# Kernel tuning notes

Measured on AMD Instinct MI355X. Metric: run time of the kernel, lower is better.

## Reference

```python
import jax, jax.numpy as jnp
import numpy as np
from jax.ops import segment_sum

N = 100000   # total nodes
M = 50000    # propagated subset size (len(index))
E = 600000   # edges over the subset graph
D = 128      # embedding_size
EPS = 1e-8
N_LAYERS = 3  # self.LayerNums


def setup_inputs() -> dict:
    key = jax.random.key(0)
    ks = jax.random.split(key, 12)
    features = jax.random.normal(ks[0], (N, D), dtype=jnp.float32)
    index = jnp.arange(M, dtype=jnp.int64)  # subset of nodes that get propagated
    edge_row = jax.random.randint(ks[1], (E,), 0, M, dtype=jnp.int64)
    edge_col = jax.random.randint(ks[2], (E,), 0, M, dtype=jnp.int64)
    edge_val = jax.random.uniform(ks[3], (E,), dtype=jnp.float32)
    # MLP prediction weights: D -> D//2 -> D//4 -> D//6 -> 1 (last no bias)
    def xavier(k, fan_in, fan_out):
        lim = jnp.sqrt(6.0 / (fan_in + fan_out)).astype(jnp.float32)
        return jax.random.uniform(k, (fan_in, fan_out), jnp.float32, -lim, lim)
    W1 = xavier(ks[4], D, D // 2); b1 = jnp.zeros((D // 2,), jnp.float32)
    W2 = xavier(ks[5], D // 2, D // 4); b2 = jnp.zeros((D // 4,), jnp.float32)
    W3 = xavier(ks[6], D // 4, D // 6); b3 = jnp.zeros((D // 6,), jnp.float32)
    W4 = xavier(ks[7], D // 6, 1)
    return {"features": features, "index": index, "edge_row": edge_row,
            "edge_col": edge_col, "edge_val": edge_val,
            "W1": W1, "b1": b1, "W2": W2, "b2": b2, "W3": W3, "b3": b3, "W4": W4}


def _gcn_layer(features, index, row, col, val):
    # symmetric normalization: d = rowsum(A)+eps; A' = d^-1/2 A d^-1/2
    deg = segment_sum(val, row, num_segments=M)
    d_inv_sqrt = jax.lax.rsqrt(deg + EPS)
    nval = val * d_inv_sqrt[row] * d_inv_sqrt[col]
    sub = features[index]                      # [M, D] subset_features
    msg = sub[col] * nval[:, None]             # [E, D]
    out = segment_sum(msg, row, num_segments=M)  # spmm -> [M, D]
    # new_features[index] = out; untouched rows keep original features
    return features.at[index].set(out)


def reference(features, index, edge_row, edge_col, edge_val,
              W1, b1, W2, b2, W3, b3, W4):
    x = features
    for _ in range(N_LAYERS):
        x = _gcn_layer(x, index, edge_row, edge_col, edge_val)
    # MLP prediction head (eval mode: dropout off), LeakyReLU slope 0.01
    h = jax.nn.leaky_relu(x @ W1 + b1, 0.01)
    h = jax.nn.leaky_relu(h @ W2 + b2, 0.01)
    h = jax.nn.leaky_relu(h @ W3 + b3, 0.01)
    return jax.nn.sigmoid(h @ W4)              # [N, 1]
```

## Files before the change

### kernel.cpp

```cpp
#include <hip/hip_runtime.h>
#include <math.h>

#define NN 100000
#define MM 50000
#define EE 600000
#define DD 128
#define NB 196
#define NNP 100096

typedef short bf16x8 __attribute__((ext_vector_type(8)));
typedef float f32x4 __attribute__((ext_vector_type(4)));

__device__ __forceinline__ float bl(unsigned u) { return __uint_as_float(u << 16); }
__device__ __forceinline__ float bh(unsigned u) { return __uint_as_float(u & 0xFFFF0000u); }
__device__ __forceinline__ unsigned rne(float f) {
    unsigned u = __float_as_uint(f);
    return (u + 0x7FFFu + ((u >> 16) & 1u)) >> 16;
}
__device__ __forceinline__ unsigned pk2(float a, float b) { return rne(a) | (rne(b) << 16); }

__device__ __forceinline__ void fmab8(float v, uint4 u, float* a) {
    a[0] = fmaf(v, bl(u.x), a[0]); a[1] = fmaf(v, bh(u.x), a[1]);
    a[2] = fmaf(v, bl(u.y), a[2]); a[3] = fmaf(v, bh(u.y), a[3]);
    a[4] = fmaf(v, bl(u.z), a[4]); a[5] = fmaf(v, bh(u.z), a[5]);
    a[6] = fmaf(v, bl(u.w), a[6]); a[7] = fmaf(v, bh(u.w), a[7]);
}

__device__ __forceinline__ void fma21(float h, const float* wrow, float* a) {
    #pragma unroll
    for (int j = 0; j < 21; ++j) a[j] = fmaf(h, wrow[j], a[j]);
}

__global__ void deg_count_kernel(const int* __restrict__ row, const float* __restrict__ val,
                                 unsigned long long* __restrict__ dcpack,
                                 int* __restrict__ slot, int* __restrict__ invidx) {
    int e = blockIdx.x * 256 + threadIdx.x;
    if (e < NN) invidx[e] = -1;
    if (e < EE) {
        int r = row[e];
        unsigned long long add = (1ULL << 44) | (unsigned long long)(val[e] * 4294967296.0f);
        unsigned long long old = atomicAdd(&dcpack[r], add);
        slot[e] = (int)(old >> 44);
    }
}

__global__ void fused_setup_kernel(const unsigned long long* __restrict__ dcpack,
                                   float* __restrict__ dis,
                                   const int* __restrict__ index, int* __restrict__ invidx,
                                   int* __restrict__ cnt, int* __restrict__ partial,
                                   int* __restrict__ bsum) {
    __shared__ int ws[4];
    int tid = threadIdx.x, lane = tid & 63, w = tid >> 6;
    int i = blockIdx.x * 256 + tid;
    int v = 0;
    if (i < MM) {
        unsigned long long pkv = dcpack[i];
        v = (int)(pkv >> 44);
        float dsum = (float)(pkv & ((1ULL << 44) - 1)) * (1.0f / 4294967296.0f);
        dis[i] = rsqrtf(dsum + 1e-8f);
        invidx[index[i]] = i;
        cnt[i] = v;
    }
    int x = v;
    #pragma unroll
    for (int off = 1; off < 64; off <<= 1) {
        int t = __shfl_up(x, off, 64);
        if (lane >= off) x += t;
    }
    if (lane == 63) ws[w] = x;
    __syncthreads();
    int add = 0;
    for (int q = 0; q < w; ++q) add += ws[q];
    x += add;
    if (i < MM) partial[i] = x;
    if (tid == 255) bsum[blockIdx.x] = x;
}

__global__ void scanB_kernel(const int* __restrict__ bsum, int* __restrict__ boff) {
    int lane = threadIdx.x;
    int carry = 0;
    for (int base = 0; base < NB; base += 64) {
        int v = (base + lane < NB) ? bsum[base + lane] : 0;
        int x = v;
        #pragma unroll
        for (int off = 1; off < 64; off <<= 1) {
            int t = __shfl_up(x, off, 64);
            if (lane >= off) x += t;
        }
        if (base + lane < NB) boff[base + lane] = carry + x - v;
        carry += __shfl(x, 63);
    }
}

__global__ void scanC_kernel(const int* __restrict__ partial, const int* __restrict__ cnt,
                             const int* __restrict__ boff, int* __restrict__ rowptr) {
    int i = blockIdx.x * 256 + threadIdx.x;
    if (i < MM) rowptr[i] = partial[i] - cnt[i] + boff[i >> 8];
    if (i == 0) rowptr[MM] = EE;
}

__global__ void scatter_kernel(const int* __restrict__ row, const int* __restrict__ col,
                               const float* __restrict__ val, const float* __restrict__ dis,
                               const int* __restrict__ rowptr, const int* __restrict__ slot,
                               int* __restrict__ col_s, float* __restrict__ val_s) {
    int e = blockIdx.x * 256 + threadIdx.x;
    if (e < EE) {
        int r = row[e], c = col[e];
        int pos = rowptr[r] + slot[e];
        col_s[pos] = c;
        val_s[pos] = val[e] * dis[r] * dis[c];
    }
}

__global__ void cvt_kernel(const float* __restrict__ feat, const int* __restrict__ index,
                           const int* __restrict__ invidx,
                           unsigned* __restrict__ X0b, unsigned* __restrict__ Xfull,
                           const float* __restrict__ W1, const float* __restrict__ W2,
                           unsigned* __restrict__ W1b, unsigned* __restrict__ W2b) {
    int i = blockIdx.x * 256 + threadIdx.x;
    int n = i >> 6, u = i & 63;
    if (n < NN && invidx[n] < 0) {
        float2 f = ((const float2*)feat)[(size_t)n * 64 + u];
        Xfull[(size_t)n * 64 + u] = pk2(f.x, f.y);
    }
    if (i < MM * 64) {
        int idx = index[n];
        float2 f = ((const float2*)feat)[(size_t)idx * 64 + u];
        X0b[i] = pk2(f.x, f.y);
    }
    if (i < 4096) {
        int j = i >> 6, kp = i & 63;
        W1b[i] = pk2(W1[(2 * kp) * 64 + j], W1[(2 * kp + 1) * 64 + j]);
    } else if (i < 5120) {
        int t = i - 4096;
        int j = t >> 5, kp = t & 31;
        W2b[t] = pk2(W2[(2 * kp) * 32 + j], W2[(2 * kp + 1) * 32 + j]);
    }
}

__global__ __launch_bounds__(256) void spmm_kernel(
    const int* __restrict__ rowptr, const int* __restrict__ cols,
    const float* __restrict__ vals, const unsigned short* __restrict__ X,
    unsigned short* __restrict__ Y, const int* __restrict__ remap) {
    int lane = threadIdx.x & 63;
    int wid = threadIdx.x >> 6;
    int g = lane >> 4, sub = lane & 15;
    int r = blockIdx.x * 16 + wid * 4 + g;
    bool valid = (r < MM);
    int rc = valid ? r : (MM - 1);
    int s = rowptr[rc], e = rowptr[rc + 1];
    const uint4* __restrict__ X4 = (const uint4*)X;
    float a[8] = {0.f, 0.f, 0.f, 0.f, 0.f, 0.f, 0.f, 0.f};
    for (int base = s; base < e; base += 16) {
        int cnt = min(16, e - base);
        int c = 0; float v = 0.f;
        if (sub < cnt) { c = cols[base + sub]; v = vals[base + sub]; }
        int j = 0;
        for (; j + 4 <= cnt; j += 4) {
            int c0 = __shfl(c, g * 16 + j);     float v0 = __shfl(v, g * 16 + j);
            int c1 = __shfl(c, g * 16 + j + 1); float v1 = __shfl(v, g * 16 + j + 1);
            int c2 = __shfl(c, g * 16 + j + 2); float v2 = __shfl(v, g * 16 + j + 2);
            int c3 = __shfl(c, g * 16 + j + 3); float v3 = __shfl(v, g * 16 + j + 3);
            uint4 u0 = X4[(size_t)c0 * 16 + sub];
            uint4 u1 = X4[(size_t)c1 * 16 + sub];
            uint4 u2 = X4[(size_t)c2 * 16 + sub];
            uint4 u3 = X4[(size_t)c3 * 16 + sub];
            fmab8(v0, u0, a);
            fmab8(v1, u1, a);
            fmab8(v2, u2, a);
            fmab8(v3, u3, a);
        }
        for (; j < cnt; ++j) {
            int cc = __shfl(c, g * 16 + j); float vv = __shfl(v, g * 16 + j);
            uint4 u0 = X4[(size_t)cc * 16 + sub];
            fmab8(vv, u0, a);
        }
    }
    if (valid) {
        int dst = remap ? remap[rc] : rc;
        uint4 o;
        o.x = pk2(a[0], a[1]); o.y = pk2(a[2], a[3]);
        o.z = pk2(a[4], a[5]); o.w = pk2(a[6], a[7]);
        ((uint4*)Y)[(size_t)dst * 16 + sub] = o;
    }
}

__global__ __launch_bounds__(256) void mlp_kernel(
    const unsigned* __restrict__ Xfull,
    const unsigned* __restrict__ W1b, const float* __restrict__ b1,
    const unsigned* __restrict__ W2b, const float* __restrict__ b2,
    const float* __restrict__ W3, const float* __restrict__ b3,
    const float* __restrict__ W4, float* __restrict__ out) {
    __shared__ float hls[4 * 1088];
    int tid = threadIdx.x;
    int lane = tid & 63, w = tid >> 6;
    int p = lane & 15, q = lane >> 4;
    float* hw = hls + w * 1088;
    int nb = blockIdx.x * 64;
    int node = nb + w * 16 + p;

    bf16x8 af[4];
    #pragma unroll
    for (int kc = 0; kc < 4; ++kc) {
        uint4 u = *(const uint4*)(Xfull + (size_t)node * 64 + kc * 16 + q * 4);
        af[kc] = *(const bf16x8*)&u;
    }
    f32x4 acc[4];
    #pragma unroll
    for (int jt = 0; jt < 4; ++jt) {
        float bv = b1[jt * 16 + p];
        acc[jt][0] = bv; acc[jt][1] = bv; acc[jt][2] = bv; acc[jt][3] = bv;
    }
    #pragma unroll
    for (int jt = 0; jt < 4; ++jt) {
        #pragma unroll
        for (int kc = 0; kc < 4; ++kc) {
            uint4 u = *(const uint4*)(W1b + (jt * 16 + p) * 64 + kc * 16 + q * 4);
            bf16x8 bf = *(const bf16x8*)&u;
            acc[jt] = __builtin_amdgcn_mfma_f32_16x16x32_bf16(af[kc], bf, acc[jt], 0, 0, 0);
        }
    }
    #pragma unroll
    for (int jt = 0; jt < 4; ++jt) {
        #pragma unroll
        for (int r = 0; r < 4; ++r) {
            float v = acc[jt][r];
            v = v > 0.f ? v : 0.01f * v;
            hw[(q * 4 + r) * 68 + jt * 16 + p] = v;
        }
    }
    bf16x8 a2f[2];
    #pragma unroll
    for (int kc = 0; kc < 2; ++kc) {
        const float* hp = hw + p * 68 + kc * 32 + q * 8;
        f32x4 v0 = *(const f32x4*)hp;
        f32x4 v1 = *(const f32x4*)(hp + 4);
        uint4 uu = make_uint4(pk2(v0[0], v0[1]), pk2(v0[2], v0[3]),
                              pk2(v1[0], v1[1]), pk2(v1[2], v1[3]));
        a2f[kc] = *(const bf16x8*)&uu;
    }
    f32x4 acc2[2];
    #pragma unroll
    for (int jt = 0; jt < 2; ++jt) {
        float bv = b2[jt * 16 + p];
        acc2[jt][0] = bv; acc2[jt][1] = bv; acc2[jt][2] = bv; acc2[jt][3] = bv;
        #pragma unroll
        for (int kc = 0; kc < 2; ++kc) {
            uint4 u = *(const uint4*)(W2b + (jt * 16 + p) * 32 + kc * 16 + q * 4);
            bf16x8 bf = *(const bf16x8*)&u;
            acc2[jt] = __builtin_amdgcn_mfma_f32_16x16x32_bf16(a2f[kc], bf, acc2[jt], 0, 0, 0);
        }
    }
    #pragma unroll
    for (int jt = 0; jt < 2; ++jt) {
        #pragma unroll
        for (int r = 0; r < 4; ++r) {
            float v = acc2[jt][r];
            v = v > 0.f ? v : 0.01f * v;
            hw[(q * 4 + r) * 36 + jt * 16 + p] = v;
        }
    }
    float a3[21];
    #pragma unroll
    for (int j = 0; j < 21; ++j) a3[j] = b3[j];
    #pragma unroll 4
    for (int k = 0; k < 32; ++k) {
        float hk = hw[p * 36 + k];
        fma21(hk, W3 + k * 21, a3);
    }
    float s = 0.f;
    #pragma unroll
    for (int j = 0; j < 21; ++j) {
        float vj = a3[j] > 0.f ? a3[j] : 0.01f * a3[j];
        s = fmaf(vj, W4[j], s);
    }
    if (q == 0) {
        int n = nb + w * 16 + p;
        if (n < NN) out[n] = 1.f / (1.f + expf(-s));
    }
}

extern "C" void kernel_launch(void* const* d_in, const int* in_sizes, int n_in,
                              void* d_out, int out_size, void* d_ws, size_t ws_size,
                              hipStream_t stream) {
    const float* feat = (const float*)d_in[0];
    const int*   index = (const int*)d_in[1];
    const int*   erow = (const int*)d_in[2];
    const int*   ecol = (const int*)d_in[3];
    const float* evalp = (const float*)d_in[4];
    const float* W1 = (const float*)d_in[5];
    const float* b1 = (const float*)d_in[6];
    const float* W2 = (const float*)d_in[7];
    const float* b2 = (const float*)d_in[8];
    const float* W3 = (const float*)d_in[9];
    const float* b3 = (const float*)d_in[10];
    const float* W4 = (const float*)d_in[11];
    float* out = (float*)d_out;

    char* ws = (char*)d_ws;
    size_t off = 0;
    auto alloc = [&](size_t bytes) -> void* {
        void* p = ws + off;
        off += (bytes + 255) & ~(size_t)255;
        return p;
    };
    unsigned long long* dcpack = (unsigned long long*)alloc((size_t)MM * 8);
    float* dis     = (float*)alloc((size_t)MM * 4);
    int*   cnt     = (int*)  alloc((size_t)MM * 4);
    int*   rowptr  = (int*)  alloc((size_t)(MM + 1) * 4);
    int*   partial = (int*)  alloc((size_t)MM * 4);
    int*   bsum    = (int*)  alloc((size_t)NB * 4);
    int*   boff    = (int*)  alloc((size_t)NB * 4);
    int*   slot    = (int*)  alloc((size_t)EE * 4);
    int*   col_s   = (int*)  alloc((size_t)EE * 4);
    float* val_s   = (float*)alloc((size_t)EE * 4);
    int*   invidx  = (int*)  alloc((size_t)NN * 4);
    unsigned* W1b  = (unsigned*)alloc(4096 * 4);
    unsigned* W2b  = (unsigned*)alloc(1024 * 4);
    unsigned*       X0b   = (unsigned*)      alloc((size_t)MM * DD * 2);
    unsigned short* Xa    = (unsigned short*)alloc((size_t)MM * DD * 2);
    unsigned short* Xb    = (unsigned short*)alloc((size_t)MM * DD * 2);
    unsigned*       Xfull = (unsigned*)      alloc((size_t)NNP * DD * 2);

    hipMemsetAsync(dcpack, 0, (size_t)MM * 8, stream);

    deg_count_kernel<<<(EE + 255) / 256, 256, 0, stream>>>(erow, evalp, dcpack, slot, invidx);
    fused_setup_kernel<<<NB, 256, 0, stream>>>(dcpack, dis, index, invidx, cnt, partial, bsum);
    scanB_kernel<<<1, 64, 0, stream>>>(bsum, boff);
    scanC_kernel<<<(MM + 255) / 256, 256, 0, stream>>>(partial, cnt, boff, rowptr);
    scatter_kernel<<<(EE + 255) / 256, 256, 0, stream>>>(erow, ecol, evalp, dis,
                                                         rowptr, slot, col_s, val_s);
    cvt_kernel<<<(NN * 64 + 255) / 256, 256, 0, stream>>>(feat, index, invidx, X0b, Xfull,
                                                          W1, W2, W1b, W2b);

    spmm_kernel<<<(MM + 15) / 16, 256, 0, stream>>>(rowptr, col_s, val_s,
                                                    (const unsigned short*)X0b, Xa, nullptr);
    spmm_kernel<<<(MM + 15) / 16, 256, 0, stream>>>(rowptr, col_s, val_s, Xa, Xb, nullptr);
    spmm_kernel<<<(MM + 15) / 16, 256, 0, stream>>>(rowptr, col_s, val_s, Xb,
                                                    (unsigned short*)Xfull, index);

    mlp_kernel<<<(NNP + 63) / 64, 256, 0, stream>>>(Xfull, W1b, b1, W2b, b2,
                                                    W3, b3, W4, out);
}
```

Baseline: 270.6 us.

## Sort rows by degree and pad CSR rows to multiples of four

Rebuilds the CSR setup as a counting sort of rows by degree, using per-block degree histograms and a bin scan. Each row's edge list is padded to a multiple of four with zeroed entries. The SpMM then handles rows in descending-degree order, so groups sharing a wavefront have similar trip counts, and it loads columns and values as int4/float4 without shuffles or tail loops. The cost is larger zero-filled edge buffers, a wider memset and an extra sort pass. Rows with degree 255 or more all share one histogram bin.

```diff
diff --git a/kernel.cpp b/kernel.cpp
--- a/kernel.cpp
+++ b/kernel.cpp
@@ -7,6 +7,7 @@
 #define DD 128
 #define NB 196
 #define NNP 100096
+#define EE4 750000
 
 typedef short bf16x8 __attribute__((ext_vector_type(8)));
 typedef float f32x4 __attribute__((ext_vector_type(4)));
@@ -47,66 +48,87 @@
 __global__ void fused_setup_kernel(const unsigned long long* __restrict__ dcpack,
                                    float* __restrict__ dis,
                                    const int* __restrict__ index, int* __restrict__ invidx,
-                                   int* __restrict__ cnt, int* __restrict__ partial,
-                                   int* __restrict__ bsum) {
-    __shared__ int ws[4];
-    int tid = threadIdx.x, lane = tid & 63, w = tid >> 6;
+                                   int* __restrict__ cnt, int* __restrict__ blockhist) {
+    __shared__ int lh[256];
+    int tid = threadIdx.x;
     int i = blockIdx.x * 256 + tid;
-    int v = 0;
+    lh[tid] = 0;
+    __syncthreads();
     if (i < MM) {
         unsigned long long pkv = dcpack[i];
-        v = (int)(pkv >> 44);
+        int v = (int)(pkv >> 44);
         float dsum = (float)(pkv & ((1ULL << 44) - 1)) * (1.0f / 4294967296.0f);
         dis[i] = rsqrtf(dsum + 1e-8f);
         invidx[index[i]] = i;
         cnt[i] = v;
-    }
-    int x = v;
-    #pragma unroll
-    for (int off = 1; off < 64; off <<= 1) {
-        int t = __shfl_up(x, off, 64);
-        if (lane >= off) x += t;
-    }
-    if (lane == 63) ws[w] = x;
+        atomicAdd(&lh[min(v, 255)], 1);
+    }
     __syncthreads();
-    int add = 0;
-    for (int q = 0; q < w; ++q) add += ws[q];
-    x += add;
-    if (i < MM) partial[i] = x;
-    if (tid == 255) bsum[blockIdx.x] = x;
-}
-
-__global__ void scanB_kernel(const int* __restrict__ bsum, int* __restrict__ boff) {
+    blockhist[tid * NB + blockIdx.x] = lh[tid];
+}
+
+__global__ void scan_bins_kernel(const int* __restrict__ blockhist,
+                                 int* __restrict__ blockoff, int* __restrict__ total) {
+    int d = blockIdx.x;
     int lane = threadIdx.x;
     int carry = 0;
     for (int base = 0; base < NB; base += 64) {
-        int v = (base + lane < NB) ? bsum[base + lane] : 0;
+        int b = base + lane;
+        int v = (b < NB) ? blockhist[d * NB + b] : 0;
         int x = v;
         #pragma unroll
         for (int off = 1; off < 64; off <<= 1) {
             int t = __shfl_up(x, off, 64);
             if (lane >= off) x += t;
         }
-        if (base + lane < NB) boff[base + lane] = carry + x - v;
+        if (b < NB) blockoff[d * NB + b] = carry + x - v;
         carry += __shfl(x, 63);
     }
-}
-
-__global__ void scanC_kernel(const int* __restrict__ partial, const int* __restrict__ cnt,
-                             const int* __restrict__ boff, int* __restrict__ rowptr) {
-    int i = blockIdx.x * 256 + threadIdx.x;
-    if (i < MM) rowptr[i] = partial[i] - cnt[i] + boff[i >> 8];
-    if (i == 0) rowptr[MM] = EE;
+    if (lane == 0) total[d] = carry;
+}
+
+__global__ void sort_rows_kernel(const int* __restrict__ cnt, const int* __restrict__ blockoff,
+                                 const int* __restrict__ total, const int* __restrict__ index,
+                                 int4* __restrict__ meta, int* __restrict__ row_s4) {
+    __shared__ int lh[256], sbin[256], spad[256], ws[8];
+    int tid = threadIdx.x, lane = tid & 63, w = tid >> 6;
+    lh[tid] = 0;
+    int t = total[tid];
+    int v1 = t, v2 = t * ((tid + 3) & ~3);
+    int x1 = v1, x2 = v2;
+    #pragma unroll
+    for (int off = 1; off < 64; off <<= 1) {
+        int t1 = __shfl_up(x1, off, 64);
+        int t2 = __shfl_up(x2, off, 64);
+        if (lane >= off) { x1 += t1; x2 += t2; }
+    }
+    if (lane == 63) { ws[w] = x1; ws[4 + w] = x2; }
+    __syncthreads();
+    int a1 = 0, a2 = 0;
+    for (int q = 0; q < w; ++q) { a1 += ws[q]; a2 += ws[4 + q]; }
+    sbin[tid] = a1 + x1 - v1;
+    spad[tid] = a2 + x2 - v2;
+    __syncthreads();
+    int i = blockIdx.x * 256 + tid;
+    if (i < MM) {
+        int d = cnt[i], c = min(d, 255);
+        int lrank = atomicAdd(&lh[c], 1);
+        int k = blockoff[c * NB + blockIdx.x] + lrank;
+        int spos = sbin[c] + k;
+        int s4 = spad[c] + k * ((d + 3) & ~3);
+        meta[MM - 1 - spos] = make_int4(s4, d, i, index[i]);
+        row_s4[i] = s4;
+    }
 }
 
 __global__ void scatter_kernel(const int* __restrict__ row, const int* __restrict__ col,
                                const float* __restrict__ val, const float* __restrict__ dis,
-                               const int* __restrict__ rowptr, const int* __restrict__ slot,
+                               const int* __restrict__ row_s4, const int* __restrict__ slot,
                                int* __restrict__ col_s, float* __restrict__ val_s) {
     int e = blockIdx.x * 256 + threadIdx.x;
     if (e < EE) {
         int r = row[e], c = col[e];
-        int pos = rowptr[r] + slot[e];
+        int pos = row_s4[r] + slot[e];
         col_s[pos] = c;
         val_s[pos] = val[e] * dis[r] * dis[c];
     }
@@ -139,49 +161,38 @@
 }
 
 __global__ __launch_bounds__(256) void spmm_kernel(
-    const int* __restrict__ rowptr, const int* __restrict__ cols,
+    const int4* __restrict__ meta, const int* __restrict__ cols,
     const float* __restrict__ vals, const unsigned short* __restrict__ X,
-    unsigned short* __restrict__ Y, const int* __restrict__ remap) {
+    unsigned short* __restrict__ Y, int use_remap) {
     int lane = threadIdx.x & 63;
     int wid = threadIdx.x >> 6;
     int g = lane >> 4, sub = lane & 15;
-    int r = blockIdx.x * 16 + wid * 4 + g;
-    bool valid = (r < MM);
-    int rc = valid ? r : (MM - 1);
-    int s = rowptr[rc], e = rowptr[rc + 1];
+    int ri = blockIdx.x * 16 + wid * 4 + g;
+    bool valid = (ri < MM);
+    int rc = valid ? ri : (MM - 1);
+    int4 mt = meta[rc];
+    int s = mt.x, d = mt.y;
     const uint4* __restrict__ X4 = (const uint4*)X;
     float a[8] = {0.f, 0.f, 0.f, 0.f, 0.f, 0.f, 0.f, 0.f};
-    for (int base = s; base < e; base += 16) {
-        int cnt = min(16, e - base);
-        int c = 0; float v = 0.f;
-        if (sub < cnt) { c = cols[base + sub]; v = vals[base + sub]; }
-        int j = 0;
-        for (; j + 4 <= cnt; j += 4) {
-            int c0 = __shfl(c, g * 16 + j);     float v0 = __shfl(v, g * 16 + j);
-            int c1 = __shfl(c, g * 16 + j + 1); float v1 = __shfl(v, g * 16 + j + 1);
-            int c2 = __shfl(c, g * 16 + j + 2); float v2 = __shfl(v, g * 16 + j + 2);
-            int c3 = __shfl(c, g * 16 + j + 3); float v3 = __shfl(v, g * 16 + j + 3);
-            uint4 u0 = X4[(size_t)c0 * 16 + sub];
-            uint4 u1 = X4[(size_t)c1 * 16 + sub];
-            uint4 u2 = X4[(size_t)c2 * 16 + sub];
-            uint4 u3 = X4[(size_t)c3 * 16 + sub];
-            fmab8(v0, u0, a);
-            fmab8(v1, u1, a);
-            fmab8(v2, u2, a);
-            fmab8(v3, u3, a);
-        }
-        for (; j < cnt; ++j) {
-            int cc = __shfl(c, g * 16 + j); float vv = __shfl(v, g * 16 + j);
-            uint4 u0 = X4[(size_t)cc * 16 + sub];
-            fmab8(vv, u0, a);
-        }
+    int e4 = s + d;
+    for (int base = s; base < e4; base += 4) {
+        int4 c4 = *(const int4*)(cols + base);
+        float4 v4 = *(const float4*)(vals + base);
+        uint4 u0 = X4[c4.x * 16 + sub];
+        uint4 u1 = X4[c4.y * 16 + sub];
+        uint4 u2 = X4[c4.z * 16 + sub];
+        uint4 u3 = X4[c4.w * 16 + sub];
+        fmab8(v4.x, u0, a);
+        fmab8(v4.y, u1, a);
+        fmab8(v4.z, u2, a);
+        fmab8(v4.w, u3, a);
     }
     if (valid) {
-        int dst = remap ? remap[rc] : rc;
+        int dst = use_remap ? mt.w : mt.z;
         uint4 o;
         o.x = pk2(a[0], a[1]); o.y = pk2(a[2], a[3]);
         o.z = pk2(a[4], a[5]); o.w = pk2(a[6], a[7]);
-        ((uint4*)Y)[(size_t)dst * 16 + sub] = o;
+        ((uint4*)Y)[dst * 16 + sub] = o;
     }
 }
 
@@ -305,16 +316,19 @@
         return p;
     };
     unsigned long long* dcpack = (unsigned long long*)alloc((size_t)MM * 8);
+    int*   col_s   = (int*)  alloc((size_t)EE4 * 4);
+    float* val_s   = (float*)alloc((size_t)EE4 * 4);
+    size_t zero_span = (size_t)((char*)val_s - (char*)dcpack) + (size_t)EE4 * 4;
+
     float* dis     = (float*)alloc((size_t)MM * 4);
     int*   cnt     = (int*)  alloc((size_t)MM * 4);
-    int*   rowptr  = (int*)  alloc((size_t)(MM + 1) * 4);
-    int*   partial = (int*)  alloc((size_t)MM * 4);
-    int*   bsum    = (int*)  alloc((size_t)NB * 4);
-    int*   boff    = (int*)  alloc((size_t)NB * 4);
     int*   slot    = (int*)  alloc((size_t)EE * 4);
-    int*   col_s   = (int*)  alloc((size_t)EE * 4);
-    float* val_s   = (float*)alloc((size_t)EE * 4);
     int*   invidx  = (int*)  alloc((size_t)NN * 4);
+    int*   row_s4  = (int*)  alloc((size_t)MM * 4);
+    int*   blockhist = (int*)alloc((size_t)256 * NB * 4);
+    int*   blockoff  = (int*)alloc((size_t)256 * NB * 4);
+    int*   total     = (int*)alloc((size_t)256 * 4);
+    int4*  meta      = (int4*)alloc((size_t)MM * 16);
     unsigned* W1b  = (unsigned*)alloc(4096 * 4);
     unsigned* W2b  = (unsigned*)alloc(1024 * 4);
     unsigned*       X0b   = (unsigned*)      alloc((size_t)MM * DD * 2);
@@ -322,22 +336,22 @@
     unsigned short* Xb    = (unsigned short*)alloc((size_t)MM * DD * 2);
     unsigned*       Xfull = (unsigned*)      alloc((size_t)NNP * DD * 2);
 
-    hipMemsetAsync(dcpack, 0, (size_t)MM * 8, stream);
+    hipMemsetAsync(dcpack, 0, zero_span, stream);
 
     deg_count_kernel<<<(EE + 255) / 256, 256, 0, stream>>>(erow, evalp, dcpack, slot, invidx);
-    fused_setup_kernel<<<NB, 256, 0, stream>>>(dcpack, dis, index, invidx, cnt, partial, bsum);
-    scanB_kernel<<<1, 64, 0, stream>>>(bsum, boff);
-    scanC_kernel<<<(MM + 255) / 256, 256, 0, stream>>>(partial, cnt, boff, rowptr);
+    fused_setup_kernel<<<NB, 256, 0, stream>>>(dcpack, dis, index, invidx, cnt, blockhist);
+    scan_bins_kernel<<<256, 64, 0, stream>>>(blockhist, blockoff, total);
+    sort_rows_kernel<<<NB, 256, 0, stream>>>(cnt, blockoff, total, index, meta, row_s4);
     scatter_kernel<<<(EE + 255) / 256, 256, 0, stream>>>(erow, ecol, evalp, dis,
-                                                         rowptr, slot, col_s, val_s);
+                                                         row_s4, slot, col_s, val_s);
     cvt_kernel<<<(NN * 64 + 255) / 256, 256, 0, stream>>>(feat, index, invidx, X0b, Xfull,
                                                           W1, W2, W1b, W2b);
 
-    spmm_kernel<<<(MM + 15) / 16, 256, 0, stream>>>(rowptr, col_s, val_s,
-                                                    (const unsigned short*)X0b, Xa, nullptr);
-    spmm_kernel<<<(MM + 15) / 16, 256, 0, stream>>>(rowptr, col_s, val_s, Xa, Xb, nullptr);
-    spmm_kernel<<<(MM + 15) / 16, 256, 0, stream>>>(rowptr, col_s, val_s, Xb,
-                                                    (unsigned short*)Xfull, index);
+    spmm_kernel<<<(MM + 15) / 16, 256, 0, stream>>>(meta, col_s, val_s,
+                                                    (const unsigned short*)X0b, Xa, 0);
+    spmm_kernel<<<(MM + 15) / 16, 256, 0, stream>>>(meta, col_s, val_s, Xa, Xb, 0);
+    spmm_kernel<<<(MM + 15) / 16, 256, 0, stream>>>(meta, col_s, val_s, Xb,
+                                                    (unsigned short*)Xfull, 1);
 
     mlp_kernel<<<(NNP + 63) / 64, 256, 0, stream>>>(Xfull, W1b, b1, W2b, b2,
                                                     W3, b3, W4, out);
```

Result: no change. 270.8 us (+0.1%).
